# Kernel tuning notes

Hardware: AMD Instinct MI355X
Metric: run time of the kernel (lower is better)

The kernel has to match this reference:

```python
import jax, jax.numpy as jnp
import numpy as np


def setup_inputs() -> dict:
    key = jax.random.key(0)
    ks = jax.random.split(key, 6)
    B, L, D, H, W = 32, 1024, 128, 128, 9
    F = D + W  # feature dim after one-hot positional embed
    rn = lambda k, shape, s: (jax.random.normal(k, shape, jnp.float32) * s)
    return {
        "embeddings": rn(ks[0], (B, L, D), 1.0),
        "masks": jnp.ones((B, L), jnp.float32),  # unused in math (as in source)
        "w1_w": rn(ks[1], (F, H), 0.05),
        "w1_b": jnp.zeros((H,), jnp.float32),
        "w2_w": rn(ks[2], (F, H), 0.05),
        "w2_b": jnp.zeros((H,), jnp.float32),
        "v_w": rn(ks[3], (H, 1), 0.05),
        "v_b": jnp.zeros((1,), jnp.float32),
        "cnn_w": rn(ks[4], (F * W, H), 0.02),
        "cnn_b": jnp.zeros((H,), jnp.float32),
        "window_size": 9,
    }


def reference(embeddings, masks, w1_w, w1_b, w2_w, w2_b, v_w, v_b, cnn_w, cnn_b, window_size):
    # Vectorized form of the per-position loop in LocalConvolutionLayer.forward.
    B, L, D = embeddings.shape
    W = window_size
    half = W // 2
    # Zero-pad then gather all sliding windows at once: [B, L, W, D]
    padded = jnp.pad(embeddings, ((0, 0), (half, half), (0, 0)))
    idx = jnp.arange(L)[:, None] + jnp.arange(W)[None, :]  # [L, W]
    win = padded[:, idx, :]
    # One-hot within-window positional embedding, concatenated on channels -> F = D + W
    pos = jnp.broadcast_to(jnp.eye(W, dtype=embeddings.dtype), (B, L, W, W))
    ctx = jnp.concatenate([win, pos], axis=-1)  # [B, L, W, F]
    ent = ctx[:, :, half, :]                    # center token, [B, L, F]
    # AttentionLayer: v(tanh(w1(ent)[:,None] + w2(ctx)))
    re = ent @ w1_w + w1_b                      # [B, L, H]
    rc = ctx @ w2_w + w2_b                      # [B, L, W, H]
    scores = jnp.tanh(re[:, :, None, :] + rc) @ v_w + v_b  # [B, L, W, 1]
    weights = jax.nn.softmax(scores, axis=2)
    out = (weights * ctx).reshape(B, L, W * ctx.shape[-1])  # [B, L, W*F]
    return out @ cnn_w + cnn_b                  # [B, L, H]
```

## Files before the change

### kernel.cpp

```cpp
#include <hip/hip_runtime.h>
#include <hip/hip_bf16.h>


typedef __attribute__((ext_vector_type(8))) short bf16x8;
typedef __attribute__((ext_vector_type(4))) float f32x4;

#define LL 1024
#define TANHK 2.885390081777927f

__device__ __forceinline__ unsigned short f2bf(float f) {
  unsigned int u = __float_as_uint(f);
  u = u + 0x7FFFu + ((u >> 16) & 1u);
  return (unsigned short)(u >> 16);
}
__device__ __forceinline__ float bf2f(unsigned short us) {
  return __uint_as_float(((unsigned int)us) << 16);
}
__device__ __forceinline__ unsigned cvt_pk_bf16(float lo, float hi) {
  unsigned r;
  asm("v_cvt_pk_bf16_f32 %0, %1, %2" : "=v"(r) : "v"(lo), "v"(hi));
  return r;
}

__global__ __launch_bounds__(256) void prep_kernel(
    const float* __restrict__ w1, const float* __restrict__ w2,
    const float* __restrict__ cnn,
    unsigned short* __restrict__ W12Frag, unsigned short* __restrict__ CwFrag) {
  int gid = blockIdx.x * 256 + threadIdx.x;
  if (blockIdx.x < 128) {
    int d = gid >> 8, n = gid & 255;
    float v = (n < 128) ? w1[d * 128 + n] : w2[d * 128 + (n - 128)];
    int tile = (n >> 4) * 4 + (d >> 5);
    int lane = ((d >> 3) & 3) * 16 + (n & 15);
    W12Frag[(tile * 64 + lane) * 8 + (d & 7)] = f2bf(v);
  } else {
    int idx = gid - 32768;
    int h = idx & 127;
    int wd = idx >> 7;
    int w = wd >> 7, d = wd & 127;
    float v = cnn[(w * 137 + d) * 128 + h];
    int tile = (w * 8 + (h >> 4)) * 4 + (d >> 5);
    int lane = ((d >> 3) & 3) * 16 + (h & 15);
    CwFrag[(tile * 64 + lane) * 8 + (d & 7)] = f2bf(v);
  }
}

__global__ __launch_bounds__(256, 4) void mega_kernel(
    const float* __restrict__ emb,
    const unsigned short* __restrict__ W12Frag,
    const unsigned short* __restrict__ CwFrag,
    const float* __restrict__ w1, const float* __restrict__ w1b,
    const float* __restrict__ w2, const float* __restrict__ w2b,
    const float* __restrict__ vw,
    const float* __restrict__ cnn, const float* __restrict__ cnnb,
    float* __restrict__ out) {
  extern __shared__ __align__(16) unsigned char smem[];
  uint4* E           = (uint4*)smem;
  unsigned short* GP = (unsigned short*)(smem + 12288);
  float* pwP         = (float*)(smem + 25344);
  float* vwP         = (float*)(smem + 29952);
  float* wtT         = (float*)(smem + 30464);

  int tid = threadIdx.x;
  int bid = blockIdx.x;
  int b = bid >> 5, l0 = (bid & 31) << 5;
  int lane = tid & 63, wid = tid >> 6;
  int l15 = lane & 15, l4 = lane >> 4;
  const bf16x8* Wf = (const bf16x8*)W12Frag;
  const bf16x8* Cf = (const bf16x8*)CwFrag;

  #pragma unroll
  for (int s = 0; s < 3; ++s) {
    int i = tid + s * 256;
    int er = i >> 4, g = i & 15;
    int t = l0 + er - 4;
    uint4 v = {0u, 0u, 0u, 0u};
    if (er < 40 && t >= 0 && t < LL) {
      const float4* src = (const float4*)(emb + ((size_t)(b * LL + t) << 7) + g * 8);
      float4 x0 = src[0], x1 = src[1];
      v.x = cvt_pk_bf16(x0.x, x0.y);
      v.y = cvt_pk_bf16(x0.z, x0.w);
      v.z = cvt_pk_bf16(x1.x, x1.y);
      v.w = cvt_pk_bf16(x1.z, x1.w);
    }
    E[er * 16 + (g ^ (er & 7))] = v;
  }
  #pragma unroll
  for (int s = 0; s < 5; ++s) {
    int i = tid + s * 256;
    if (i < 1152) {
      int w = i >> 7, p = i & 127;
      int h = ((p & 7) << 4) + (p >> 3);
      pwP[i] = TANHK * (w2[(128 + w) * 128 + h] + w2b[h] +
                        w1[132 * 128 + h] + w1b[h]);
    } else {
      int p = i - 1152;
      int h = ((p & 7) << 4) + (p >> 3);
      vwP[p] = vw[h];
    }
  }
  __syncthreads();

  const bf16x8* Eb = (const bf16x8*)E;
  f32x4 af[8];
  #pragma unroll
  for (int nn = 0; nn < 8; ++nn) af[nn] = (f32x4){0.f, 0.f, 0.f, 0.f};
  {
    int er0f = 4 + ((wid & 1) << 4);
    #pragma unroll
    for (int kk = 0; kk < 4; ++kk) {
      int gk = kk * 4 + l4;
      int er = er0f + l15;
      bf16x8 aF = Eb[er * 16 + (gk ^ (er & 7))];
      #pragma unroll
      for (int nn = 0; nn < 8; ++nn) {
        bf16x8 bF = Wf[(nn * 4 + kk) * 64 + lane];
        af[nn] = __builtin_amdgcn_mfma_f32_16x16x32_bf16(aF, bF, af[nn], 0, 0, 0);
      }
    }
  }
  if (wid < 3) {
    int er0g = wid << 4;
    f32x4 ag[8];
    #pragma unroll
    for (int nn = 0; nn < 8; ++nn) ag[nn] = (f32x4){0.f, 0.f, 0.f, 0.f};
    #pragma unroll
    for (int kk = 0; kk < 4; ++kk) {
      int gk = kk * 4 + l4;
      int er = er0g + l15;
      bf16x8 aF = Eb[er * 16 + (gk ^ (er & 7))];
      #pragma unroll
      for (int nn = 0; nn < 8; ++nn) {
        bf16x8 bF = Wf[((8 + nn) * 4 + kk) * 64 + lane];
        ag[nn] = __builtin_amdgcn_mfma_f32_16x16x32_bf16(aF, bF, ag[nn], 0, 0, 0);
      }
    }
    #pragma unroll
    for (int j = 0; j < 4; ++j) {
      int row = er0g + l4 * 4 + j;
      uint4 v;
      v.x = cvt_pk_bf16(TANHK * ag[0][j], TANHK * ag[1][j]);
      v.y = cvt_pk_bf16(TANHK * ag[2][j], TANHK * ag[3][j]);
      v.z = cvt_pk_bf16(TANHK * ag[4][j], TANHK * ag[5][j]);
      v.w = cvt_pk_bf16(TANHK * ag[6][j], TANHK * ag[7][j]);
      *(uint4*)(GP + row * 136 + l15 * 8) = v;
    }
  }
  __syncthreads();

  {
    int rbase = (wid & 1) << 4;
    f32x4 vr0 = *(const f32x4*)(vwP + l15 * 8);
    f32x4 vr1 = *(const f32x4*)(vwP + l15 * 8 + 4);

#define DO_SCORE(J)                                                            \
    {                                                                          \
      int rl = rbase + l4 * 4 + (J);                                           \
      float sc[9];                                                             \
      _Pragma("unroll")                                                        \
      for (int w = 0; w < 9; ++w) {                                            \
        bf16x8 graw = *(const bf16x8*)(GP + (rl + w) * 136 + l15 * 8);         \
        f32x4 pw0 = *(const f32x4*)(pwP + w * 128 + l15 * 8);                  \
        f32x4 pw1 = *(const f32x4*)(pwP + w * 128 + l15 * 8 + 4);              \
        float a = 0.f;                                                         \
        _Pragma("unroll")                                                      \
        for (int c = 0; c < 4; ++c) {                                          \
          float e = exp2f(fmaf(af[c][(J)], TANHK,                              \
                               bf2f((unsigned short)graw[c]) + pw0[c]));       \
          a = fmaf(vr0[c], __builtin_amdgcn_rcpf(1.f + e), a);                 \
        }                                                                      \
        _Pragma("unroll")                                                      \
        for (int c = 0; c < 4; ++c) {                                          \
          float e = exp2f(fmaf(af[4 + c][(J)], TANHK,                          \
                               bf2f((unsigned short)graw[4 + c]) + pw1[c]));   \
          a = fmaf(vr1[c], __builtin_amdgcn_rcpf(1.f + e), a);                 \
        }                                                                      \
        a += __shfl_xor(a, 1, 64);                                             \
        a += __shfl_xor(a, 2, 64);                                             \
        a += __shfl_xor(a, 4, 64);                                             \
        a += __shfl_xor(a, 8, 64);                                             \
        sc[w] = a;                                                             \
      }                                                                        \
      float mn = sc[0];                                                        \
      _Pragma("unroll")                                                        \
      for (int w = 1; w < 9; ++w) mn = fminf(mn, sc[w]);                       \
      float pp[9], sum = 0.f;                                                  \
      _Pragma("unroll")                                                        \
      for (int w = 0; w < 9; ++w) { pp[w] = exp2f(TANHK * (mn - sc[w])); sum += pp[w]; } \
      float inv = __builtin_amdgcn_rcpf(sum);                                  \
      if (l15 < 9) {                                                           \
        float wv = pp[0];                                                      \
        _Pragma("unroll")                                                      \
        for (int w = 1; w < 9; ++w) wv = (l15 == w) ? pp[w] : wv;              \
        wtT[l15 * 36 + rl] = wv * inv;                                         \
      }                                                                        \
    }

    if (!(wid & 2)) { DO_SCORE(0); DO_SCORE(1); }
    else            { DO_SCORE(2); DO_SCORE(3); }
#undef DO_SCORE
  }
  __syncthreads();

  int h0 = (wid << 5) + l15;
  f32x4 fin[2][2];
  #pragma unroll
  for (int m = 0; m < 2; ++m)
    #pragma unroll
    for (int n = 0; n < 2; ++n) fin[m][n] = (f32x4){0.f, 0.f, 0.f, 0.f};
  #pragma unroll
  for (int w = 0; w < 9; ++w) {
    f32x4 tmp[2][2];
    #pragma unroll
    for (int m = 0; m < 2; ++m)
      #pragma unroll
      for (int n = 0; n < 2; ++n) tmp[m][n] = (f32x4){0.f, 0.f, 0.f, 0.f};
    #pragma unroll
    for (int kk = 0; kk < 4; ++kk) {
      int gk = kk * 4 + l4;
      bf16x8 aF[2];
      #pragma unroll
      for (int m = 0; m < 2; ++m) {
        int er = m * 16 + l15 + w;
        aF[m] = Eb[er * 16 + (gk ^ (er & 7))];
      }
      #pragma unroll
      for (int n = 0; n < 2; ++n) {
        bf16x8 bF = Cf[((w * 8 + (wid << 1) + n) * 4 + kk) * 64 + lane];
        #pragma unroll
        for (int m = 0; m < 2; ++m)
          tmp[m][n] = __builtin_amdgcn_mfma_f32_16x16x32_bf16(aF[m], bF, tmp[m][n], 0, 0, 0);
      }
    }
    float cp0 = cnn[(w * 138 + 128) * 128 + h0];
    float cp1 = cnn[(w * 138 + 128) * 128 + h0 + 16];
    #pragma unroll
    for (int m = 0; m < 2; ++m) {
      f32x4 wt4 = *(const f32x4*)(wtT + w * 36 + m * 16 + l4 * 4);
      #pragma unroll
      for (int j = 0; j < 4; ++j) {
        fin[m][0][j] += wt4[j] * (tmp[m][0][j] + cp0);
        fin[m][1][j] += wt4[j] * (tmp[m][1][j] + cp1);
      }
    }
  }
  float cb0 = cnnb[h0], cb1 = cnnb[h0 + 16];
  #pragma unroll
  for (int m = 0; m < 2; ++m)
    #pragma unroll
    for (int j = 0; j < 4; ++j) {
      int r = m * 16 + l4 * 4 + j;
      size_t o = ((size_t)(b * LL + l0 + r) << 7) + h0;
      out[o]      = fin[m][0][j] + cb0;
      out[o + 16] = fin[m][1][j] + cb1;
    }
}

extern "C" void kernel_launch(void* const* d_in, const int* in_sizes, int n_in,
                              void* d_out, int out_size, void* d_ws, size_t ws_size,
                              hipStream_t stream) {
  const float* emb  = (const float*)d_in[0];
  const float* w1   = (const float*)d_in[2];
  const float* w1b  = (const float*)d_in[3];
  const float* w2   = (const float*)d_in[4];
  const float* w2b  = (const float*)d_in[5];
  const float* vw   = (const float*)d_in[6];
  const float* cnn  = (const float*)d_in[8];
  const float* cnnb = (const float*)d_in[9];
  float* out = (float*)d_out;

  char* ws = (char*)d_ws;
  unsigned short* W12Frag = (unsigned short*)(ws);
  unsigned short* CwFrag  = (unsigned short*)(ws + 65536);

  prep_kernel<<<704, 256, 0, stream>>>(w1, w2, cnn, W12Frag, CwFrag);
  mega_kernel<<<1024, 256, 31760, stream>>>(emb, W12Frag, CwFrag, w1, w1b, w2, w2b,
                                            vw, cnn, cnnb, out);
}
```

Baseline: 132.7 us.

## Split fused mega kernel into projection, softmax-weight, and output kernels

The single fused kernel is replaced by three kernels. The first computes both bf16 projections (center and context) once per row into a global FG buffer, which removes the redundant halo recompute of G. The second computes attention scores and softmax weights into a global weight array, and the third does the CNN output GEMM. This lowers per-kernel register and LDS pressure and avoids recomputation, at the cost of extra global memory round-trips (an 8 MB FG buffer plus weights) and additional launches.

```diff
diff --git a/kernel.cpp b/kernel.cpp
--- a/kernel.cpp
+++ b/kernel.cpp
@@ -45,28 +45,156 @@
   }
 }
 
-__global__ __launch_bounds__(256, 4) void mega_kernel(
-    const float* __restrict__ emb,
-    const unsigned short* __restrict__ W12Frag,
-    const unsigned short* __restrict__ CwFrag,
+__global__ __launch_bounds__(64, 8) void fg_kernel(
+    const float* __restrict__ emb, const unsigned short* __restrict__ W12Frag,
+    unsigned short* __restrict__ FG) {
+  int bid = blockIdx.x;
+  int part = bid & 1;
+  int r0 = (bid >> 1) << 5;
+  int lane = threadIdx.x;
+  int l15 = lane & 15, l4 = lane >> 4;
+  const bf16x8* Wf = (const bf16x8*)W12Frag;
+
+  f32x4 acc[2][8];
+  #pragma unroll
+  for (int m = 0; m < 2; ++m)
+    #pragma unroll
+    for (int nn = 0; nn < 8; ++nn) acc[m][nn] = (f32x4){0.f, 0.f, 0.f, 0.f};
+
+  #pragma unroll
+  for (int kk = 0; kk < 4; ++kk) {
+    bf16x8 aF[2];
+    #pragma unroll
+    for (int m = 0; m < 2; ++m) {
+      const float4* src = (const float4*)(emb +
+          (size_t)(r0 + m * 16 + l15) * 128 + kk * 32 + l4 * 8);
+      float4 x0 = src[0], x1 = src[1];
+      uint4 v;
+      v.x = cvt_pk_bf16(x0.x, x0.y);
+      v.y = cvt_pk_bf16(x0.z, x0.w);
+      v.z = cvt_pk_bf16(x1.x, x1.y);
+      v.w = cvt_pk_bf16(x1.z, x1.w);
+      aF[m] = *(bf16x8*)&v;
+    }
+    #pragma unroll
+    for (int nn = 0; nn < 8; ++nn) {
+      bf16x8 bF = Wf[((part * 8 + nn) * 4 + kk) * 64 + lane];
+      #pragma unroll
+      for (int m = 0; m < 2; ++m)
+        acc[m][nn] = __builtin_amdgcn_mfma_f32_16x16x32_bf16(aF[m], bF, acc[m][nn], 0, 0, 0);
+    }
+  }
+  #pragma unroll
+  for (int m = 0; m < 2; ++m)
+    #pragma unroll
+    for (int j = 0; j < 4; ++j) {
+      int row = r0 + m * 16 + l4 * 4 + j;
+      uint4 v;
+      v.x = cvt_pk_bf16(TANHK * acc[m][0][j], TANHK * acc[m][1][j]);
+      v.y = cvt_pk_bf16(TANHK * acc[m][2][j], TANHK * acc[m][3][j]);
+      v.z = cvt_pk_bf16(TANHK * acc[m][4][j], TANHK * acc[m][5][j]);
+      v.w = cvt_pk_bf16(TANHK * acc[m][6][j], TANHK * acc[m][7][j]);
+      *(uint4*)(FG + (size_t)row * 256 + part * 128 + l15 * 8) = v;
+    }
+}
+
+__global__ __launch_bounds__(256, 4) void wt_kernel(
+    const unsigned short* __restrict__ FG,
     const float* __restrict__ w1, const float* __restrict__ w1b,
     const float* __restrict__ w2, const float* __restrict__ w2b,
-    const float* __restrict__ vw,
-    const float* __restrict__ cnn, const float* __restrict__ cnnb,
-    float* __restrict__ out) {
-  extern __shared__ __align__(16) unsigned char smem[];
-  uint4* E           = (uint4*)smem;
-  unsigned short* GP = (unsigned short*)(smem + 12288);
-  float* pwP         = (float*)(smem + 25344);
-  float* vwP         = (float*)(smem + 29952);
-  float* wtT         = (float*)(smem + 30464);
-
+    const float* __restrict__ vw, float* __restrict__ wtT) {
+  __shared__ float pwP[1152];
+  __shared__ float vwP[128];
+  int tid = threadIdx.x;
+  #pragma unroll
+  for (int s = 0; s < 5; ++s) {
+    int i = tid + s * 256;
+    if (i < 1152) {
+      int w = i >> 7, p = i & 127;
+      int h = ((p & 7) << 4) + (p >> 3);
+      pwP[i] = TANHK * (w2[(128 + w) * 128 + h] + w2b[h] +
+                        w1[132 * 128 + h] + w1b[h]);
+    } else if (i < 1280) {
+      int p = i - 1152;
+      int h = ((p & 7) << 4) + (p >> 3);
+      vwP[p] = vw[h];
+    }
+  }
+  __syncthreads();
+
+  int r0 = blockIdx.x << 5;
+  int gb = r0 & ~1023;
+  int lc0 = r0 & 1023;
+  int lane = tid & 63, wid = tid >> 6;
+  int l15 = lane & 15, l4 = lane >> 4;
+  int u8 = l15 * 8;
+  int rbase = (wid & 1) << 4;
+  f32x4 vr0 = *(const f32x4*)(vwP + u8);
+  f32x4 vr1 = *(const f32x4*)(vwP + u8 + 4);
+  const bf16x8 gz = {0, 0, 0, 0, 0, 0, 0, 0};
+
+#define DO_SCORE(J)                                                            \
+  {                                                                            \
+    int rl = rbase + l4 * 4 + (J);                                             \
+    int row = r0 + rl, lcol = lc0 + rl;                                        \
+    bf16x8 fraw = *(const bf16x8*)(FG + (size_t)row * 256 + u8);               \
+    float sc[9];                                                               \
+    _Pragma("unroll")                                                          \
+    for (int w = 0; w < 9; ++w) {                                              \
+      int t = lcol + w - 4;                                                    \
+      bf16x8 graw = (t >= 0 && t < LL)                                         \
+          ? *(const bf16x8*)(FG + (size_t)(gb + t) * 256 + 128 + u8) : gz;     \
+      f32x4 pw0 = *(const f32x4*)(pwP + w * 128 + u8);                         \
+      f32x4 pw1 = *(const f32x4*)(pwP + w * 128 + u8 + 4);                     \
+      float a = 0.f;                                                           \
+      _Pragma("unroll")                                                        \
+      for (int c = 0; c < 4; ++c) {                                            \
+        float e = exp2f(bf2f((unsigned short)fraw[c]) +                        \
+                        bf2f((unsigned short)graw[c]) + pw0[c]);               \
+        a = fmaf(vr0[c], __builtin_amdgcn_rcpf(1.f + e), a);                   \
+      }                                                                        \
+      _Pragma("unroll")                                                        \
+      for (int c = 0; c < 4; ++c) {                                            \
+        float e = exp2f(bf2f((unsigned short)fraw[4 + c]) +                    \
+                        bf2f((unsigned short)graw[4 + c]) + pw1[c]);           \
+        a = fmaf(vr1[c], __builtin_amdgcn_rcpf(1.f + e), a);                   \
+      }                                                                        \
+      a += __shfl_xor(a, 1, 64);                                               \
+      a += __shfl_xor(a, 2, 64);                                               \
+      a += __shfl_xor(a, 4, 64);                                               \
+      a += __shfl_xor(a, 8, 64);                                               \
+      sc[w] = a;                                                               \
+    }                                                                          \
+    float mn = sc[0];                                                          \
+    _Pragma("unroll")                                                          \
+    for (int w = 1; w < 9; ++w) mn = fminf(mn, sc[w]);                         \
+    float pp[9], sum = 0.f;                                                    \
+    _Pragma("unroll")                                                          \
+    for (int w = 0; w < 9; ++w) { pp[w] = exp2f(TANHK * (mn - sc[w])); sum += pp[w]; } \
+    float inv = __builtin_amdgcn_rcpf(sum);                                    \
+    if (l15 < 9) {                                                             \
+      float wv = pp[0];                                                        \
+      _Pragma("unroll")                                                        \
+      for (int w = 1; w < 9; ++w) wv = (l15 == w) ? pp[w] : wv;                \
+      wtT[l15 * 32768 + row] = wv * inv;                                       \
+    }                                                                          \
+  }
+
+  if (!(wid & 2)) { DO_SCORE(0); DO_SCORE(1); }
+  else            { DO_SCORE(2); DO_SCORE(3); }
+#undef DO_SCORE
+}
+
+__global__ __launch_bounds__(256, 4) void out_kernel(
+    const float* __restrict__ emb, const unsigned short* __restrict__ CwFrag,
+    const float* __restrict__ wtT, const float* __restrict__ cnn,
+    const float* __restrict__ cnnb, float* __restrict__ out) {
+  __shared__ uint4 E[48 * 16];
   int tid = threadIdx.x;
   int bid = blockIdx.x;
   int b = bid >> 5, l0 = (bid & 31) << 5;
   int lane = tid & 63, wid = tid >> 6;
   int l15 = lane & 15, l4 = lane >> 4;
-  const bf16x8* Wf = (const bf16x8*)W12Frag;
   const bf16x8* Cf = (const bf16x8*)CwFrag;
 
   #pragma unroll
@@ -85,123 +213,9 @@
     }
     E[er * 16 + (g ^ (er & 7))] = v;
   }
-  #pragma unroll
-  for (int s = 0; s < 5; ++s) {
-    int i = tid + s * 256;
-    if (i < 1152) {
-      int w = i >> 7, p = i & 127;
-      int h = ((p & 7) << 4) + (p >> 3);
-      pwP[i] = TANHK * (w2[(128 + w) * 128 + h] + w2b[h] +
-                        w1[132 * 128 + h] + w1b[h]);
-    } else {
-      int p = i - 1152;
-      int h = ((p & 7) << 4) + (p >> 3);
-      vwP[p] = vw[h];
-    }
-  }
   __syncthreads();
 
   const bf16x8* Eb = (const bf16x8*)E;
-  f32x4 af[8];
-  #pragma unroll
-  for (int nn = 0; nn < 8; ++nn) af[nn] = (f32x4){0.f, 0.f, 0.f, 0.f};
-  {
-    int er0f = 4 + ((wid & 1) << 4);
-    #pragma unroll
-    for (int kk = 0; kk < 4; ++kk) {
-      int gk = kk * 4 + l4;
-      int er = er0f + l15;
-      bf16x8 aF = Eb[er * 16 + (gk ^ (er & 7))];
-      #pragma unroll
-      for (int nn = 0; nn < 8; ++nn) {
-        bf16x8 bF = Wf[(nn * 4 + kk) * 64 + lane];
-        af[nn] = __builtin_amdgcn_mfma_f32_16x16x32_bf16(aF, bF, af[nn], 0, 0, 0);
-      }
-    }
-  }
-  if (wid < 3) {
-    int er0g = wid << 4;
-    f32x4 ag[8];
-    #pragma unroll
-    for (int nn = 0; nn < 8; ++nn) ag[nn] = (f32x4){0.f, 0.f, 0.f, 0.f};
-    #pragma unroll
-    for (int kk = 0; kk < 4; ++kk) {
-      int gk = kk * 4 + l4;
-      int er = er0g + l15;
-      bf16x8 aF = Eb[er * 16 + (gk ^ (er & 7))];
-      #pragma unroll
-      for (int nn = 0; nn < 8; ++nn) {
-        bf16x8 bF = Wf[((8 + nn) * 4 + kk) * 64 + lane];
-        ag[nn] = __builtin_amdgcn_mfma_f32_16x16x32_bf16(aF, bF, ag[nn], 0, 0, 0);
-      }
-    }
-    #pragma unroll
-    for (int j = 0; j < 4; ++j) {
-      int row = er0g + l4 * 4 + j;
-      uint4 v;
-      v.x = cvt_pk_bf16(TANHK * ag[0][j], TANHK * ag[1][j]);
-      v.y = cvt_pk_bf16(TANHK * ag[2][j], TANHK * ag[3][j]);
-      v.z = cvt_pk_bf16(TANHK * ag[4][j], TANHK * ag[5][j]);
-      v.w = cvt_pk_bf16(TANHK * ag[6][j], TANHK * ag[7][j]);
-      *(uint4*)(GP + row * 136 + l15 * 8) = v;
-    }
-  }
-  __syncthreads();
-
-  {
-    int rbase = (wid & 1) << 4;
-    f32x4 vr0 = *(const f32x4*)(vwP + l15 * 8);
-    f32x4 vr1 = *(const f32x4*)(vwP + l15 * 8 + 4);
-
-#define DO_SCORE(J)                                                            \
-    {                                                                          \
-      int rl = rbase + l4 * 4 + (J);                                           \
-      float sc[9];                                                             \
-      _Pragma("unroll")                                                        \
-      for (int w = 0; w < 9; ++w) {                                            \
-        bf16x8 graw = *(const bf16x8*)(GP + (rl + w) * 136 + l15 * 8);         \
-        f32x4 pw0 = *(const f32x4*)(pwP + w * 128 + l15 * 8);                  \
-        f32x4 pw1 = *(const f32x4*)(pwP + w * 128 + l15 * 8 + 4);              \
-        float a = 0.f;                                                         \
-        _Pragma("unroll")                                                      \
-        for (int c = 0; c < 4; ++c) {                                          \
-          float e = exp2f(fmaf(af[c][(J)], TANHK,                              \
-                               bf2f((unsigned short)graw[c]) + pw0[c]));       \
-          a = fmaf(vr0[c], __builtin_amdgcn_rcpf(1.f + e), a);                 \
-        }                                                                      \
-        _Pragma("unroll")                                                      \
-        for (int c = 0; c < 4; ++c) {                                          \
-          float e = exp2f(fmaf(af[4 + c][(J)], TANHK,                          \
-                               bf2f((unsigned short)graw[4 + c]) + pw1[c]));   \
-          a = fmaf(vr1[c], __builtin_amdgcn_rcpf(1.f + e), a);                 \
-        }                                                                      \
-        a += __shfl_xor(a, 1, 64);                                             \
-        a += __shfl_xor(a, 2, 64);                                             \
-        a += __shfl_xor(a, 4, 64);                                             \
-        a += __shfl_xor(a, 8, 64);                                             \
-        sc[w] = a;                                                             \
-      }                                                                        \
-      float mn = sc[0];                                                        \
-      _Pragma("unroll")                                                        \
-      for (int w = 1; w < 9; ++w) mn = fminf(mn, sc[w]);                       \
-      float pp[9], sum = 0.f;                                                  \
-      _Pragma("unroll")                                                        \
-      for (int w = 0; w < 9; ++w) { pp[w] = exp2f(TANHK * (mn - sc[w])); sum += pp[w]; } \
-      float inv = __builtin_amdgcn_rcpf(sum);                                  \
-      if (l15 < 9) {                                                           \
-        float wv = pp[0];                                                      \
-        _Pragma("unroll")                                                      \
-        for (int w = 1; w < 9; ++w) wv = (l15 == w) ? pp[w] : wv;              \
-        wtT[l15 * 36 + rl] = wv * inv;                                         \
-      }                                                                        \
-    }
-
-    if (!(wid & 2)) { DO_SCORE(0); DO_SCORE(1); }
-    else            { DO_SCORE(2); DO_SCORE(3); }
-#undef DO_SCORE
-  }
-  __syncthreads();
-
   int h0 = (wid << 5) + l15;
   f32x4 fin[2][2];
   #pragma unroll
@@ -236,7 +250,7 @@
     float cp1 = cnn[(w * 138 + 128) * 128 + h0 + 16];
     #pragma unroll
     for (int m = 0; m < 2; ++m) {
-      f32x4 wt4 = *(const f32x4*)(wtT + w * 36 + m * 16 + l4 * 4);
+      f32x4 wt4 = *(const f32x4*)(wtT + w * 32768 + (bid << 5) + m * 16 + l4 * 4);
       #pragma unroll
       for (int j = 0; j < 4; ++j) {
         fin[m][0][j] += wt4[j] * (tmp[m][0][j] + cp0);
@@ -272,8 +286,11 @@
   char* ws = (char*)d_ws;
   unsigned short* W12Frag = (unsigned short*)(ws);
   unsigned short* CwFrag  = (unsigned short*)(ws + 65536);
+  float* wtT              = (float*)(ws + 360448);
+  unsigned short* FG      = (unsigned short*)(ws + 1540096);
 
   prep_kernel<<<704, 256, 0, stream>>>(w1, w2, cnn, W12Frag, CwFrag);
-  mega_kernel<<<1024, 256, 31760, stream>>>(emb, W12Frag, CwFrag, w1, w1b, w2, w2b,
-                                            vw, cnn, cnnb, out);
-}
+  fg_kernel<<<2048, 64, 0, stream>>>(emb, W12Frag, FG);
+  wt_kernel<<<1024, 256, 0, stream>>>(FG, w1, w1b, w2, w2b, vw, wtT);
+  out_kernel<<<1024, 256, 0, stream>>>(emb, CwFrag, wtT, cnn, cnnb, out);
+}
```

After: 166.8 us. 1.26x slower.

## Double tile size to 64 rows per block with 512 threads and prefetched weights

Applied to the files above, without the earlier changes.

Each block now handles 64 sequence positions with 8 waves instead of 32 positions with 4 waves. This cuts the halo overhead on the embedding window and the redundant per-block setup of position and v-weight tables. The final conv GEMM double-buffers the weight fragments, loading the next window's fragments while the current one's MFMAs run, and MFMA sections are wrapped in s_setprio. In exchange the kernel uses more shared memory and registers per block, so fewer blocks fit on each CU and there are only 512 blocks to spread across the device.

```diff
diff --git a/kernel.cpp b/kernel.cpp
--- a/kernel.cpp
+++ b/kernel.cpp
@@ -45,7 +45,7 @@
   }
 }
 
-__global__ __launch_bounds__(256, 4) void mega_kernel(
+__global__ __launch_bounds__(512, 4) void mega_kernel(
     const float* __restrict__ emb,
     const unsigned short* __restrict__ W12Frag,
     const unsigned short* __restrict__ CwFrag,
@@ -56,45 +56,43 @@
     float* __restrict__ out) {
   extern __shared__ __align__(16) unsigned char smem[];
   uint4* E           = (uint4*)smem;
-  unsigned short* GP = (unsigned short*)(smem + 12288);
-  float* pwP         = (float*)(smem + 25344);
-  float* vwP         = (float*)(smem + 29952);
-  float* wtT         = (float*)(smem + 30464);
+  unsigned short* GP = (unsigned short*)(smem + 20480);
+  float* pwP         = (float*)(smem + 42240);
+  float* vwP         = (float*)(smem + 46848);
+  float* wtT         = (float*)(smem + 47360);
 
   int tid = threadIdx.x;
   int bid = blockIdx.x;
-  int b = bid >> 5, l0 = (bid & 31) << 5;
+  int b = bid >> 4, l0 = (bid & 15) << 6;
   int lane = tid & 63, wid = tid >> 6;
   int l15 = lane & 15, l4 = lane >> 4;
   const bf16x8* Wf = (const bf16x8*)W12Frag;
   const bf16x8* Cf = (const bf16x8*)CwFrag;
 
   #pragma unroll
-  for (int s = 0; s < 3; ++s) {
-    int i = tid + s * 256;
-    int er = i >> 4, g = i & 15;
-    int t = l0 + er - 4;
-    uint4 v = {0u, 0u, 0u, 0u};
-    if (er < 40 && t >= 0 && t < LL) {
-      const float4* src = (const float4*)(emb + ((size_t)(b * LL + t) << 7) + g * 8);
-      float4 x0 = src[0], x1 = src[1];
-      v.x = cvt_pk_bf16(x0.x, x0.y);
-      v.y = cvt_pk_bf16(x0.z, x0.w);
-      v.z = cvt_pk_bf16(x1.x, x1.y);
-      v.w = cvt_pk_bf16(x1.z, x1.w);
-    }
-    E[er * 16 + (g ^ (er & 7))] = v;
-  }
-  #pragma unroll
   for (int s = 0; s < 5; ++s) {
-    int i = tid + s * 256;
-    if (i < 1152) {
-      int w = i >> 7, p = i & 127;
+    int i = tid + s * 512;
+    if (i < 1280) {
+      int er = i >> 4, g = i & 15;
+      int t = l0 + er - 4;
+      uint4 v = {0u, 0u, 0u, 0u};
+      if (er < 72 && t >= 0 && t < LL) {
+        const float4* src = (const float4*)(emb + ((size_t)(b * LL + t) << 7) + g * 8);
+        float4 x0 = src[0], x1 = src[1];
+        v.x = cvt_pk_bf16(x0.x, x0.y);
+        v.y = cvt_pk_bf16(x0.z, x0.w);
+        v.z = cvt_pk_bf16(x1.x, x1.y);
+        v.w = cvt_pk_bf16(x1.z, x1.w);
+      }
+      E[er * 16 + (g ^ (er & 7))] = v;
+    } else if (i < 2432) {
+      int idx = i - 1280;
+      int w = idx >> 7, p = idx & 127;
       int h = ((p & 7) << 4) + (p >> 3);
-      pwP[i] = TANHK * (w2[(128 + w) * 128 + h] + w2b[h] +
-                        w1[132 * 128 + h] + w1b[h]);
+      pwP[idx] = TANHK * (w2[(128 + w) * 128 + h] + w2b[h] +
+                          w1[132 * 128 + h] + w1b[h]);
     } else {
-      int p = i - 1152;
+      int p = i - 2432;
       int h = ((p & 7) << 4) + (p >> 3);
       vwP[p] = vw[h];
     }
@@ -106,7 +104,8 @@
   #pragma unroll
   for (int nn = 0; nn < 8; ++nn) af[nn] = (f32x4){0.f, 0.f, 0.f, 0.f};
   {
-    int er0f = 4 + ((wid & 1) << 4);
+    int er0f = 4 + ((wid & 3) << 4);
+    __builtin_amdgcn_s_setprio(1);
     #pragma unroll
     for (int kk = 0; kk < 4; ++kk) {
       int gk = kk * 4 + l4;
@@ -118,12 +117,14 @@
         af[nn] = __builtin_amdgcn_mfma_f32_16x16x32_bf16(aF, bF, af[nn], 0, 0, 0);
       }
     }
-  }
-  if (wid < 3) {
+    __builtin_amdgcn_s_setprio(0);
+  }
+  if (wid < 5) {
     int er0g = wid << 4;
     f32x4 ag[8];
     #pragma unroll
     for (int nn = 0; nn < 8; ++nn) ag[nn] = (f32x4){0.f, 0.f, 0.f, 0.f};
+    __builtin_amdgcn_s_setprio(1);
     #pragma unroll
     for (int kk = 0; kk < 4; ++kk) {
       int gk = kk * 4 + l4;
@@ -135,6 +136,7 @@
         ag[nn] = __builtin_amdgcn_mfma_f32_16x16x32_bf16(aF, bF, ag[nn], 0, 0, 0);
       }
     }
+    __builtin_amdgcn_s_setprio(0);
     #pragma unroll
     for (int j = 0; j < 4; ++j) {
       int row = er0g + l4 * 4 + j;
@@ -149,9 +151,10 @@
   __syncthreads();
 
   {
-    int rbase = (wid & 1) << 4;
-    f32x4 vr0 = *(const f32x4*)(vwP + l15 * 8);
-    f32x4 vr1 = *(const f32x4*)(vwP + l15 * 8 + 4);
+    int rbase = (wid & 3) << 4;
+    int u8 = l15 * 8;
+    f32x4 vr0 = *(const f32x4*)(vwP + u8);
+    f32x4 vr1 = *(const f32x4*)(vwP + u8 + 4);
 
 #define DO_SCORE(J)                                                            \
     {                                                                          \
@@ -159,9 +162,9 @@
       float sc[9];                                                             \
       _Pragma("unroll")                                                        \
       for (int w = 0; w < 9; ++w) {                                            \
-        bf16x8 graw = *(const bf16x8*)(GP + (rl + w) * 136 + l15 * 8);         \
-        f32x4 pw0 = *(const f32x4*)(pwP + w * 128 + l15 * 8);                  \
-        f32x4 pw1 = *(const f32x4*)(pwP + w * 128 + l15 * 8 + 4);              \
+        bf16x8 graw = *(const bf16x8*)(GP + (rl + w) * 136 + u8);              \
+        f32x4 pw0 = *(const f32x4*)(pwP + w * 128 + u8);                       \
+        f32x4 pw1 = *(const f32x4*)(pwP + w * 128 + u8 + 4);                   \
         float a = 0.f;                                                         \
         _Pragma("unroll")                                                      \
         for (int c = 0; c < 4; ++c) {                                          \
@@ -192,68 +195,79 @@
         float wv = pp[0];                                                      \
         _Pragma("unroll")                                                      \
         for (int w = 1; w < 9; ++w) wv = (l15 == w) ? pp[w] : wv;              \
-        wtT[l15 * 36 + rl] = wv * inv;                                         \
+        wtT[l15 * 68 + rl] = wv * inv;                                         \
       }                                                                        \
     }
 
-    if (!(wid & 2)) { DO_SCORE(0); DO_SCORE(1); }
+    if (!(wid & 4)) { DO_SCORE(0); DO_SCORE(1); }
     else            { DO_SCORE(2); DO_SCORE(3); }
 #undef DO_SCORE
   }
   __syncthreads();
 
-  int h0 = (wid << 5) + l15;
-  f32x4 fin[2][2];
-  #pragma unroll
-  for (int m = 0; m < 2; ++m)
-    #pragma unroll
-    for (int n = 0; n < 2; ++n) fin[m][n] = (f32x4){0.f, 0.f, 0.f, 0.f};
-  #pragma unroll
-  for (int w = 0; w < 9; ++w) {
-    f32x4 tmp[2][2];
-    #pragma unroll
-    for (int m = 0; m < 2; ++m)
-      #pragma unroll
-      for (int n = 0; n < 2; ++n) tmp[m][n] = (f32x4){0.f, 0.f, 0.f, 0.f};
-    #pragma unroll
-    for (int kk = 0; kk < 4; ++kk) {
-      int gk = kk * 4 + l4;
-      bf16x8 aF[2];
-      #pragma unroll
-      for (int m = 0; m < 2; ++m) {
-        int er = m * 16 + l15 + w;
-        aF[m] = Eb[er * 16 + (gk ^ (er & 7))];
-      }
-      #pragma unroll
-      for (int n = 0; n < 2; ++n) {
-        bf16x8 bF = Cf[((w * 8 + (wid << 1) + n) * 4 + kk) * 64 + lane];
-        #pragma unroll
-        for (int m = 0; m < 2; ++m)
-          tmp[m][n] = __builtin_amdgcn_mfma_f32_16x16x32_bf16(aF[m], bF, tmp[m][n], 0, 0, 0);
-      }
-    }
-    float cp0 = cnn[(w * 138 + 128) * 128 + h0];
-    float cp1 = cnn[(w * 138 + 128) * 128 + h0 + 16];
-    #pragma unroll
-    for (int m = 0; m < 2; ++m) {
-      f32x4 wt4 = *(const f32x4*)(wtT + w * 36 + m * 16 + l4 * 4);
-      #pragma unroll
-      for (int j = 0; j < 4; ++j) {
-        fin[m][0][j] += wt4[j] * (tmp[m][0][j] + cp0);
-        fin[m][1][j] += wt4[j] * (tmp[m][1][j] + cp1);
-      }
-    }
-  }
+  int wr = wid >> 2, wc = wid & 3;
+  int h0 = (wc << 5) + l15;
+  f32x4 fin00 = {0.f,0.f,0.f,0.f}, fin01 = {0.f,0.f,0.f,0.f};
+  f32x4 fin10 = {0.f,0.f,0.f,0.f}, fin11 = {0.f,0.f,0.f,0.f};
+  bf16x8 bufA[4][2], bufB[4][2];
+
+#define LOADB(BUF, W)                                                          \
+  _Pragma("unroll")                                                            \
+  for (int kk = 0; kk < 4; ++kk)                                               \
+    _Pragma("unroll")                                                          \
+    for (int n = 0; n < 2; ++n)                                                \
+      BUF[kk][n] = Cf[(((W) * 8 + (wc << 1) + n) * 4 + kk) * 64 + lane];
+
+#define STEP(W, CUR, NXT)                                                      \
+  {                                                                            \
+    if ((W) < 8) { LOADB(NXT, (W) + 1); }                                      \
+    f32x4 t00 = {0.f,0.f,0.f,0.f}, t01 = {0.f,0.f,0.f,0.f};                    \
+    f32x4 t10 = {0.f,0.f,0.f,0.f}, t11 = {0.f,0.f,0.f,0.f};                    \
+    __builtin_amdgcn_s_setprio(1);                                             \
+    _Pragma("unroll")                                                          \
+    for (int kk = 0; kk < 4; ++kk) {                                           \
+      int gk = kk * 4 + l4;                                                    \
+      int er0 = wr * 32 + l15 + (W);                                           \
+      int er1 = er0 + 16;                                                      \
+      bf16x8 a0 = Eb[er0 * 16 + (gk ^ (er0 & 7))];                             \
+      bf16x8 a1 = Eb[er1 * 16 + (gk ^ (er1 & 7))];                             \
+      t00 = __builtin_amdgcn_mfma_f32_16x16x32_bf16(a0, CUR[kk][0], t00, 0, 0, 0); \
+      t10 = __builtin_amdgcn_mfma_f32_16x16x32_bf16(a1, CUR[kk][0], t10, 0, 0, 0); \
+      t01 = __builtin_amdgcn_mfma_f32_16x16x32_bf16(a0, CUR[kk][1], t01, 0, 0, 0); \
+      t11 = __builtin_amdgcn_mfma_f32_16x16x32_bf16(a1, CUR[kk][1], t11, 0, 0, 0); \
+    }                                                                          \
+    __builtin_amdgcn_s_setprio(0);                                             \
+    float cp0 = cnn[((W) * 138 + 128) * 128 + h0];                             \
+    float cp1 = cnn[((W) * 138 + 128) * 128 + h0 + 16];                        \
+    f32x4 wa = *(const f32x4*)(wtT + (W) * 68 + wr * 32 + l4 * 4);             \
+    f32x4 wb = *(const f32x4*)(wtT + (W) * 68 + wr * 32 + 16 + l4 * 4);        \
+    _Pragma("unroll")                                                          \
+    for (int j = 0; j < 4; ++j) {                                              \
+      fin00[j] += wa[j] * (t00[j] + cp0);                                      \
+      fin01[j] += wa[j] * (t01[j] + cp1);                                      \
+      fin10[j] += wb[j] * (t10[j] + cp0);                                      \
+      fin11[j] += wb[j] * (t11[j] + cp1);                                      \
+    }                                                                          \
+  }
+
+  LOADB(bufA, 0);
+  STEP(0, bufA, bufB); STEP(1, bufB, bufA); STEP(2, bufA, bufB);
+  STEP(3, bufB, bufA); STEP(4, bufA, bufB); STEP(5, bufB, bufA);
+  STEP(6, bufA, bufB); STEP(7, bufB, bufA); STEP(8, bufA, bufB);
+#undef STEP
+#undef LOADB
+
   float cb0 = cnnb[h0], cb1 = cnnb[h0 + 16];
   #pragma unroll
-  for (int m = 0; m < 2; ++m)
-    #pragma unroll
-    for (int j = 0; j < 4; ++j) {
-      int r = m * 16 + l4 * 4 + j;
-      size_t o = ((size_t)(b * LL + l0 + r) << 7) + h0;
-      out[o]      = fin[m][0][j] + cb0;
-      out[o + 16] = fin[m][1][j] + cb1;
-    }
+  for (int j = 0; j < 4; ++j) {
+    int r0 = wr * 32 + l4 * 4 + j;
+    size_t o0 = ((size_t)(b * LL + l0 + r0) << 7) + h0;
+    out[o0]      = fin00[j] + cb0;
+    out[o0 + 16] = fin01[j] + cb1;
+    size_t o1 = ((size_t)(b * LL + l0 + r0 + 16) << 7) + h0;
+    out[o1]      = fin10[j] + cb0;
+    out[o1 + 16] = fin11[j] + cb1;
+  }
 }
 
 extern "C" void kernel_launch(void* const* d_in, const int* in_sizes, int n_in,
@@ -274,6 +288,6 @@
   unsigned short* CwFrag  = (unsigned short*)(ws + 65536);
 
   prep_kernel<<<704, 256, 0, stream>>>(w1, w2, cnn, W12Frag, CwFrag);
-  mega_kernel<<<1024, 256, 31760, stream>>>(emb, W12Frag, CwFrag, w1, w1b, w2, w2b,
-                                            vw, cnn, cnnb, out);
-}
+  mega_kernel<<<512, 512, 49808, stream>>>(emb, W12Frag, CwFrag, w1, w1b, w2, w2b,
+                                           vw, cnn, cnnb, out);
+}
```

Measured after the change: 124.8 us. -6.0%, faster.
